# Performance work log

Hardware: AMD Instinct MI355X
Metric: run time of the kernel (lower is better)

The kernel has to match this reference:

```python
import jax, jax.numpy as jnp
import numpy as np

N_EXPERTS = 8
N_SHARED = 1
N_ROUTED = N_EXPERTS - N_SHARED          # 7
TOP_K_ROUTED = 3 - N_SHARED              # 2 routed experts per token
C = 1024
H = 4 * C


def _mlp(x, w_fc, w_proj):
    # x: [n, C]; w_fc: [C, H]; w_proj: [H, C]; exact (erf) GELU like torch nn.GELU
    return jax.nn.gelu(x @ w_fc, approximate=False) @ w_proj


def setup_inputs() -> dict:
    key = jax.random.key(0)
    ks = jax.random.split(key, 6)
    s = 0.02
    return {
        "x": jax.random.normal(ks[0], (4, 2048, C), dtype=jnp.float32),
        "gate_w": jax.random.normal(ks[1], (N_ROUTED, C), dtype=jnp.float32) * s,
        "lb_bias": jnp.zeros((N_ROUTED,), dtype=jnp.float32),
        "shared_wfc": jax.random.normal(ks[2], (C, H), dtype=jnp.float32) * s,
        "shared_wproj": jax.random.normal(ks[3], (H, C), dtype=jnp.float32) * s,
        "routed_wfc": jax.random.normal(ks[4], (N_ROUTED, C, H), dtype=jnp.float32) * s,
        "routed_wproj": jax.random.normal(ks[5], (N_ROUTED, H, C), dtype=jnp.float32) * s,
    }


def reference(x, gate_w, lb_bias, shared_wfc, shared_wproj, routed_wfc, routed_wproj):
    B, T, Cc = x.shape
    xt = x.reshape(-1, Cc)                       # [n, C]
    n = xt.shape[0]

    # shared expert(s) applied to every token
    shared_out = _mlp(xt, shared_wfc, shared_wproj)

    # routing
    routed_logits = xt @ gate_w.T                # [n, E_r]
    sel_logits = routed_logits + lb_bias
    _, topk_idx = jax.lax.top_k(sel_logits, TOP_K_ROUTED)   # [n, k]
    routed_probs = jax.nn.softmax(routed_logits.astype(jnp.float32), axis=-1)
    topk_w = jnp.take_along_axis(routed_probs, topk_idx, axis=-1)  # [n, k]

    # per-token combine weights over routed experts: [n, E_r]
    cw = jnp.zeros((n, N_ROUTED), dtype=jnp.float32)
    cw = cw.at[jnp.arange(n)[:, None], topk_idx].add(topk_w)

    # dispatch-combine: small fixed loop over routed experts
    routed_out = jnp.zeros_like(xt)
    for e in range(N_ROUTED):
        y = _mlp(xt, routed_wfc[e], routed_wproj[e])
        routed_out = routed_out + cw[:, e:e + 1] * y

    return (shared_out + routed_out).reshape(B, T, Cc)
```

## Files before the change

kernel.cpp:

```cpp
#include <hip/hip_runtime.h>
#include <hip/hip_bf16.h>

#define AS1 __attribute__((address_space(1)))
#define AS3 __attribute__((address_space(3)))

typedef __bf16 bf16x8 __attribute__((ext_vector_type(8)));
typedef float f32x4 __attribute__((ext_vector_type(4)));

static constexpr int C_DIM = 1024;
static constexpr int H_DIM = 4096;
static constexpr int NTOK  = 8192;
static constexpr int NR    = 7;
static constexpr int NSLOT = 17408;
static constexpr int MAXT  = 136;
static constexpr size_t WSZ = (size_t)C_DIM * H_DIM;

static __device__ __forceinline__ unsigned short f2bf(float f) {
  __hip_bfloat16 h = __float2bfloat16(f);
  return *reinterpret_cast<unsigned short*>(&h);
}
static __device__ __forceinline__ float bf2f(unsigned short u) {
  unsigned int v = ((unsigned int)u) << 16;
  return *reinterpret_cast<float*>(&v);
}

static __device__ __forceinline__ float gelu_fast(float v) {
  const float u2 = -2.0f * v * (0.7978845608f + 0.0356774081f * v * v);
  return v * __builtin_amdgcn_rcpf(1.0f + __expf(u2));
}

static __device__ __forceinline__ void gload16(const void* g, void* lds) {
  __builtin_amdgcn_global_load_lds((const AS1 void*)g, (AS3 void*)lds, 16, 0, 0);
}

__global__ __launch_bounds__(256) void cast_x_kernel(const float* __restrict__ x,
                                                     unsigned short* __restrict__ xb) {
  size_t i = ((size_t)blockIdx.x * blockDim.x + threadIdx.x) * 4;
  float4 v = *(const float4*)(x + i);
  ushort4 o;
  o.x = f2bf(v.x); o.y = f2bf(v.y); o.z = f2bf(v.z); o.w = f2bf(v.w);
  *(ushort4*)(xb + i) = o;
}

__global__ __launch_bounds__(256) void init_kernel(int* __restrict__ idx, int* __restrict__ cnt,
                                                   int* __restrict__ cursor) {
  int i = blockIdx.x * 256 + threadIdx.x;
  if (i < NSLOT) idx[i] = 0;
  if (blockIdx.x == 0 && threadIdx.x < 8) { cnt[threadIdx.x] = 0; cursor[threadIdx.x] = 0; }
}

__global__ __launch_bounds__(256) void routing_kernel(const float* __restrict__ x,
                                                      const float* __restrict__ gw,
                                                      const float* __restrict__ bias,
                                                      float* __restrict__ cw,
                                                      int* __restrict__ cnt) {
  int wid = (int)((blockIdx.x * (size_t)blockDim.x + threadIdx.x) >> 6);
  int lane = threadIdx.x & 63;
  if (wid >= NTOK) return;
  const float* xt = x + (size_t)wid * C_DIM;
  float p[NR] = {0.f, 0.f, 0.f, 0.f, 0.f, 0.f, 0.f};
  for (int i = lane; i < C_DIM; i += 64) {
    float xv = xt[i];
#pragma unroll
    for (int e = 0; e < NR; ++e) p[e] += xv * gw[e * C_DIM + i];
  }
#pragma unroll
  for (int e = 0; e < NR; ++e) {
#pragma unroll
    for (int off = 32; off; off >>= 1) p[e] += __shfl_down(p[e], off);
  }
  if (lane == 0) {
    float m = p[0];
#pragma unroll
    for (int e = 1; e < NR; ++e) m = fmaxf(m, p[e]);
    float pr[NR], s = 0.f;
#pragma unroll
    for (int e = 0; e < NR; ++e) { pr[e] = __expf(p[e] - m); s += pr[e]; }
    float inv = 1.0f / s;
#pragma unroll
    for (int e = 0; e < NR; ++e) pr[e] *= inv;
    float sel[NR];
#pragma unroll
    for (int e = 0; e < NR; ++e) sel[e] = p[e] + bias[e];
    int i1 = 0;
#pragma unroll
    for (int e = 1; e < NR; ++e) if (sel[e] > sel[i1]) i1 = e;
    int i2 = -1;
#pragma unroll
    for (int e = 0; e < NR; ++e) {
      if (e == i1) continue;
      if (i2 < 0 || sel[e] > sel[i2]) i2 = e;
    }
    float c[NR] = {0.f, 0.f, 0.f, 0.f, 0.f, 0.f, 0.f};
    c[i1] = pr[i1];
    c[i2] += pr[i2];
#pragma unroll
    for (int e = 0; e < NR; ++e) cw[(size_t)wid * NR + e] = c[e];
    atomicAdd(&cnt[i1], 1);
    atomicAdd(&cnt[i2], 1);
  }
}

__global__ void scan_kernel(const int* __restrict__ cnt, int* __restrict__ offs,
                            int* __restrict__ tmap, int* __restrict__ ntiles) {
  int o = 0, nt = 0;
  for (int e = 0; e < NR; ++e) {
    offs[e] = o;
    int n = (cnt[e] + 127) & ~127;
    o += n;
    for (int tm = 0; tm < n; tm += 128) tmap[nt++] = (e << 16) | tm;
  }
  *ntiles = nt;
}

__global__ __launch_bounds__(256) void place_kernel(const float* __restrict__ cw,
                                                    const int* __restrict__ offs,
                                                    int* __restrict__ cursor,
                                                    int* __restrict__ idx,
                                                    int* __restrict__ tok2slot,
                                                    float* __restrict__ tok2w) {
  int t = blockIdx.x * 256 + threadIdx.x;
  if (t >= NTOK) return;
  int k = 0;
#pragma unroll
  for (int e = 0; e < NR; ++e) {
    float w = cw[(size_t)t * NR + e];
    if (w > 0.f) {
      int p = atomicAdd(&cursor[e], 1);
      int slot = offs[e] + p;
      idx[slot] = t;
      tok2slot[t * 2 + k] = slot;
      tok2w[t * 2 + k] = w;
      ++k;
    }
  }
}

__global__ void transpose_cast_all(const float* __restrict__ shared_w,
                                   const float* __restrict__ routed_w,
                                   unsigned short* __restrict__ out, int R, int S) {
  int e = blockIdx.z;
  const float* in = (e == 0) ? shared_w : routed_w + (size_t)(e - 1) * R * S;
  unsigned short* o = out + (size_t)e * R * S;
  __shared__ float t[32][33];
  int bx = blockIdx.x * 32;
  int by = blockIdx.y * 32;
  int tx = threadIdx.x, ty = threadIdx.y;
#pragma unroll
  for (int i = 0; i < 32; i += 8)
    t[ty + i][tx] = in[(size_t)(by + ty + i) * S + bx + tx];
  __syncthreads();
#pragma unroll
  for (int i = 0; i < 32; i += 8)
    o[(size_t)(bx + ty + i) * R + by + tx] = f2bf(t[tx][ty + i]);
}


template <bool GATHER>
__global__ __launch_bounds__(256) void gemm_fc(const unsigned short* __restrict__ A,
                                               const unsigned short* __restrict__ BtAll,
                                               unsigned short* __restrict__ Y,
                                               const int* __restrict__ idx,
                                               const int* __restrict__ offs,
                                               const int* __restrict__ tmap,
                                               const int* __restrict__ ntiles) {
  __shared__ __align__(16) unsigned short As[3][4096];
  __shared__ __align__(16) unsigned short Bs[3][4096];
  const int tid = threadIdx.x;
  const int wave = tid >> 6, lane = tid & 63;
  constexpr int NT = C_DIM / 32;

  const int f = blockIdx.y * gridDim.x + blockIdx.x;
  const int cpx = (gridDim.x * gridDim.y) >> 3;
  const int swz = (f & 7) * cpx + (f >> 3);
  const int bx = swz % gridDim.x, ty = swz / gridDim.x;

  int m0, n0, base;
  const unsigned short* Bt;
  if (GATHER) {
    if (ty >= *ntiles) return;
    const int packed = tmap[ty];
    const int e = packed >> 16;
    m0 = packed & 0xffff;
    n0 = bx * 128;
    base = offs[e];
    Bt = BtAll + (size_t)(e + 1) * WSZ;
  } else {
    m0 = ty * 128;
    n0 = bx * 128;
    base = 0;
    Bt = BtAll;
  }

  const int q0 = wave * 128 + lane, q1 = q0 + 64;
  const int kg0 = q0 >> 7, r0 = q0 & 127;
  const int kg1 = q1 >> 7, r1 = q1 & 127;
  const size_t rowA0 = GATHER ? (size_t)idx[base + m0 + r0] : (size_t)(m0 + r0);
  const size_t rowA1 = GATHER ? (size_t)idx[base + m0 + r1] : (size_t)(m0 + r1);
  const unsigned short* gA0 = A + rowA0 * C_DIM + kg0 * 8;
  const unsigned short* gA1 = A + rowA1 * C_DIM + kg1 * 8;
  const unsigned short* gB0 = Bt + (size_t)(n0 + r0) * C_DIM + kg0 * 8;
  const unsigned short* gB1 = Bt + (size_t)(n0 + r1) * C_DIM + kg1 * 8;
  const int c0 = (wave * 2 + 0) * 512, c1 = (wave * 2 + 1) * 512;

  const int wr = wave >> 1, wc = wave & 1;
  const int fr = lane & 15, fq = lane >> 4;
  f32x4 acc[4][4] = {};

  asm volatile("s_waitcnt vmcnt(0)" ::: "memory");
  gload16(gA0, &As[0][c0]); gload16(gA1, &As[0][c1]);
  gload16(gB0, &Bs[0][c0]); gload16(gB1, &Bs[0][c1]);
  gload16(gA0 + 32, &As[1][c0]); gload16(gA1 + 32, &As[1][c1]);
  gload16(gB0 + 32, &Bs[1][c0]); gload16(gB1 + 32, &Bs[1][c1]);

  int rb = 0;
  for (int t = 0; t < NT; ++t) {
    if (t + 2 < NT) {
      const int wb = (rb >= 1) ? rb - 1 : 2;
      const int nk = (t + 2) * 32;
      gload16(gA0 + nk, &As[wb][c0]); gload16(gA1 + nk, &As[wb][c1]);
      gload16(gB0 + nk, &Bs[wb][c0]); gload16(gB1 + nk, &Bs[wb][c1]);
      asm volatile("s_waitcnt vmcnt(8)" ::: "memory");
    } else if (t + 1 < NT) {
      asm volatile("s_waitcnt vmcnt(4)" ::: "memory");
    } else {
      asm volatile("s_waitcnt vmcnt(0)" ::: "memory");
    }
    __builtin_amdgcn_s_barrier();
    bf16x8 af[4], bfr[4];
#pragma unroll
    for (int m = 0; m < 4; ++m)
      af[m] = *(const bf16x8*)&As[rb][fq * 1024 + (wr * 64 + m * 16 + fr) * 8];
#pragma unroll
    for (int n = 0; n < 4; ++n)
      bfr[n] = *(const bf16x8*)&Bs[rb][fq * 1024 + (wc * 64 + n * 16 + fr) * 8];
#pragma unroll
    for (int m = 0; m < 4; ++m)
#pragma unroll
      for (int n = 0; n < 4; ++n)
        acc[m][n] = __builtin_amdgcn_mfma_f32_16x16x32_bf16(af[m], bfr[n], acc[m][n], 0, 0, 0);
    __builtin_amdgcn_s_barrier();
    rb = (rb == 2) ? 0 : rb + 1;
  }

#pragma unroll
  for (int m = 0; m < 4; ++m)
#pragma unroll
    for (int n = 0; n < 4; ++n)
#pragma unroll
      for (int j = 0; j < 4; ++j) {
        const int row = m0 + wr * 64 + m * 16 + fq * 4 + j;
        const int col = n0 + wc * 64 + n * 16 + fr;
        const float g = gelu_fast(acc[m][n][j]);
        __builtin_nontemporal_store(f2bf(g), &Y[(size_t)(base + row) * H_DIM + col]);
      }
}

__global__ __launch_bounds__(256) void gemm_proj_shared(const unsigned short* __restrict__ Yg,
                                                        const unsigned short* __restrict__ Bt,
                                                        float* __restrict__ Out) {
  __shared__ __align__(16) unsigned short As[3][4096];
  __shared__ __align__(16) unsigned short Bs[3][4096];
  const int tid = threadIdx.x;
  const int wave = tid >> 6, lane = tid & 63;
  constexpr int NT = H_DIM / 32;

  const int f = blockIdx.y * gridDim.x + blockIdx.x;
  const int cpx = (gridDim.x * gridDim.y) >> 3;
  const int swz = (f & 7) * cpx + (f >> 3);
  const int m0 = (swz / gridDim.x) * 128;
  const int n0 = (swz % gridDim.x) * 128;

  const int q0 = wave * 128 + lane, q1 = q0 + 64;
  const int kg0 = q0 >> 7, r0 = q0 & 127;
  const int kg1 = q1 >> 7, r1 = q1 & 127;
  const unsigned short* gA0 = Yg + (size_t)(m0 + r0) * H_DIM + kg0 * 8;
  const unsigned short* gA1 = Yg + (size_t)(m0 + r1) * H_DIM + kg1 * 8;
  const unsigned short* gB0 = Bt + (size_t)(n0 + r0) * H_DIM + kg0 * 8;
  const unsigned short* gB1 = Bt + (size_t)(n0 + r1) * H_DIM + kg1 * 8;
  const int c0 = (wave * 2 + 0) * 512, c1 = (wave * 2 + 1) * 512;

  const int wr = wave >> 1, wc = wave & 1;
  const int fr = lane & 15, fq = lane >> 4;
  f32x4 acc[4][4] = {};

  gload16(gA0, &As[0][c0]); gload16(gA1, &As[0][c1]);
  gload16(gB0, &Bs[0][c0]); gload16(gB1, &Bs[0][c1]);
  gload16(gA0 + 32, &As[1][c0]); gload16(gA1 + 32, &As[1][c1]);
  gload16(gB0 + 32, &Bs[1][c0]); gload16(gB1 + 32, &Bs[1][c1]);

  int rb = 0;
  for (int t = 0; t < NT; ++t) {
    if (t + 2 < NT) {
      const int wb = (rb >= 1) ? rb - 1 : 2;
      const int nk = (t + 2) * 32;
      gload16(gA0 + nk, &As[wb][c0]); gload16(gA1 + nk, &As[wb][c1]);
      gload16(gB0 + nk, &Bs[wb][c0]); gload16(gB1 + nk, &Bs[wb][c1]);
      asm volatile("s_waitcnt vmcnt(8)" ::: "memory");
    } else if (t + 1 < NT) {
      asm volatile("s_waitcnt vmcnt(4)" ::: "memory");
    } else {
      asm volatile("s_waitcnt vmcnt(0)" ::: "memory");
    }
    __builtin_amdgcn_s_barrier();
    bf16x8 af[4], bfr[4];
#pragma unroll
    for (int m = 0; m < 4; ++m)
      af[m] = *(const bf16x8*)&As[rb][fq * 1024 + (wr * 64 + m * 16 + fr) * 8];
#pragma unroll
    for (int n = 0; n < 4; ++n)
      bfr[n] = *(const bf16x8*)&Bs[rb][fq * 1024 + (wc * 64 + n * 16 + fr) * 8];
#pragma unroll
    for (int m = 0; m < 4; ++m)
#pragma unroll
      for (int n = 0; n < 4; ++n)
        acc[m][n] = __builtin_amdgcn_mfma_f32_16x16x32_bf16(af[m], bfr[n], acc[m][n], 0, 0, 0);
    __builtin_amdgcn_s_barrier();
    rb = (rb == 2) ? 0 : rb + 1;
  }

#pragma unroll
  for (int m = 0; m < 4; ++m)
#pragma unroll
    for (int n = 0; n < 4; ++n)
#pragma unroll
      for (int j = 0; j < 4; ++j) {
        const int p = wr * 64 + m * 16 + fq * 4 + j;
        const int col = n0 + wc * 64 + n * 16 + fr;
        Out[(size_t)(m0 + p) * C_DIM + col] = acc[m][n][j];
      }
}

__global__ __launch_bounds__(256) void gemm_proj_routed(const unsigned short* __restrict__ Yg,
                                                        const unsigned short* __restrict__ BtAll,
                                                        unsigned short* __restrict__ Pb,
                                                        const int* __restrict__ offs,
                                                        const int* __restrict__ tmap,
                                                        const int* __restrict__ ntiles) {
  __shared__ __align__(16) unsigned short As[3][4096];
  __shared__ __align__(16) unsigned short Bs[3][4096];
  const int tid = threadIdx.x;
  const int wave = tid >> 6, lane = tid & 63;
  constexpr int KSEG = H_DIM / 2;
  constexpr int NT = KSEG / 32;
  const int kbase = blockIdx.z * KSEG;

  const int f = blockIdx.y * gridDim.x + blockIdx.x;
  const int cpx = (gridDim.x * gridDim.y) >> 3;
  const int swz = (f & 7) * cpx + (f >> 3);
  const int bx = swz % gridDim.x, ty = swz / gridDim.x;

  if (ty >= *ntiles) return;
  const int packed = tmap[ty];
  const int e = packed >> 16;
  const int m0 = packed & 0xffff;
  const int n0 = bx * 128;
  const int base = offs[e];
  const unsigned short* Bt = BtAll + (size_t)(e + 1) * WSZ;

  const int q0 = wave * 128 + lane, q1 = q0 + 64;
  const int kg0 = q0 >> 7, r0 = q0 & 127;
  const int kg1 = q1 >> 7, r1 = q1 & 127;
  const unsigned short* gA0 = Yg + (size_t)(base + m0 + r0) * H_DIM + kbase + kg0 * 8;
  const unsigned short* gA1 = Yg + (size_t)(base + m0 + r1) * H_DIM + kbase + kg1 * 8;
  const unsigned short* gB0 = Bt + (size_t)(n0 + r0) * H_DIM + kbase + kg0 * 8;
  const unsigned short* gB1 = Bt + (size_t)(n0 + r1) * H_DIM + kbase + kg1 * 8;
  const int c0 = (wave * 2 + 0) * 512, c1 = (wave * 2 + 1) * 512;

  const int wr = wave >> 1, wc = wave & 1;
  const int fr = lane & 15, fq = lane >> 4;
  f32x4 acc[4][4] = {};

  gload16(gA0, &As[0][c0]); gload16(gA1, &As[0][c1]);
  gload16(gB0, &Bs[0][c0]); gload16(gB1, &Bs[0][c1]);
  gload16(gA0 + 32, &As[1][c0]); gload16(gA1 + 32, &As[1][c1]);
  gload16(gB0 + 32, &Bs[1][c0]); gload16(gB1 + 32, &Bs[1][c1]);

  int rb = 0;
  for (int t = 0; t < NT; ++t) {
    if (t + 2 < NT) {
      const int wb = (rb >= 1) ? rb - 1 : 2;
      const int nk = (t + 2) * 32;
      gload16(gA0 + nk, &As[wb][c0]); gload16(gA1 + nk, &As[wb][c1]);
      gload16(gB0 + nk, &Bs[wb][c0]); gload16(gB1 + nk, &Bs[wb][c1]);
      asm volatile("s_waitcnt vmcnt(8)" ::: "memory");
    } else if (t + 1 < NT) {
      asm volatile("s_waitcnt vmcnt(4)" ::: "memory");
    } else {
      asm volatile("s_waitcnt vmcnt(0)" ::: "memory");
    }
    __builtin_amdgcn_s_barrier();
    bf16x8 af[4], bfr[4];
#pragma unroll
    for (int m = 0; m < 4; ++m)
      af[m] = *(const bf16x8*)&As[rb][fq * 1024 + (wr * 64 + m * 16 + fr) * 8];
#pragma unroll
    for (int n = 0; n < 4; ++n)
      bfr[n] = *(const bf16x8*)&Bs[rb][fq * 1024 + (wc * 64 + n * 16 + fr) * 8];
#pragma unroll
    for (int m = 0; m < 4; ++m)
#pragma unroll
      for (int n = 0; n < 4; ++n)
        acc[m][n] = __builtin_amdgcn_mfma_f32_16x16x32_bf16(af[m], bfr[n], acc[m][n], 0, 0, 0);
    __builtin_amdgcn_s_barrier();
    rb = (rb == 2) ? 0 : rb + 1;
  }

#pragma unroll
  for (int m = 0; m < 4; ++m)
#pragma unroll
    for (int n = 0; n < 4; ++n)
#pragma unroll
      for (int j = 0; j < 4; ++j) {
        const int p = wr * 64 + m * 16 + fq * 4 + j;
        const int col = n0 + wc * 64 + n * 16 + fr;
        __builtin_nontemporal_store(
            f2bf(acc[m][n][j]),
            &Pb[((size_t)blockIdx.z * NSLOT + base + m0 + p) * C_DIM + col]);
      }
}

__global__ __launch_bounds__(256) void combine_kernel(const unsigned short* __restrict__ P,
                                                      const int* __restrict__ tok2slot,
                                                      const float* __restrict__ tok2w,
                                                      float* __restrict__ out) {
  const int t = blockIdx.x;
  const int c = threadIdx.x * 4;
  const int s0 = tok2slot[t * 2], s1 = tok2slot[t * 2 + 1];
  const float w0 = tok2w[t * 2], w1 = tok2w[t * 2 + 1];
  const ushort4 a0 = *(const ushort4*)&P[((size_t)0 * NSLOT + s0) * C_DIM + c];
  const ushort4 a1 = *(const ushort4*)&P[((size_t)1 * NSLOT + s0) * C_DIM + c];
  const ushort4 b0 = *(const ushort4*)&P[((size_t)0 * NSLOT + s1) * C_DIM + c];
  const ushort4 b1 = *(const ushort4*)&P[((size_t)1 * NSLOT + s1) * C_DIM + c];
  float4 o = *(float4*)&out[(size_t)t * C_DIM + c];
  o.x += w0 * (bf2f(a0.x) + bf2f(a1.x)) + w1 * (bf2f(b0.x) + bf2f(b1.x));
  o.y += w0 * (bf2f(a0.y) + bf2f(a1.y)) + w1 * (bf2f(b0.y) + bf2f(b1.y));
  o.z += w0 * (bf2f(a0.z) + bf2f(a1.z)) + w1 * (bf2f(b0.z) + bf2f(b1.z));
  o.w += w0 * (bf2f(a0.w) + bf2f(a1.w)) + w1 * (bf2f(b0.w) + bf2f(b1.w));
  *(float4*)&out[(size_t)t * C_DIM + c] = o;
}

extern "C" void kernel_launch(void* const* d_in, const int* in_sizes, int n_in,
                              void* d_out, int out_size, void* d_ws, size_t ws_size,
                              hipStream_t stream) {
  const float* x            = (const float*)d_in[0];
  const float* gate_w       = (const float*)d_in[1];
  const float* lb_bias      = (const float*)d_in[2];
  const float* shared_wfc   = (const float*)d_in[3];
  const float* shared_wproj = (const float*)d_in[4];
  const float* routed_wfc   = (const float*)d_in[5];
  const float* routed_wproj = (const float*)d_in[6];
  float* out = (float*)d_out;

  char* ws = (char*)d_ws;
  unsigned short* xb     = (unsigned short*)(ws);
  unsigned short* wfcT   = (unsigned short*)(ws + 16777216);
  unsigned short* Pb     = (unsigned short*)(ws);
  unsigned short* wprojT = (unsigned short*)(ws + 83886080);
  unsigned short* Yg     = (unsigned short*)(ws + 150994944);
  float*          cw     = (float*)(ws + 293601280);
  int*            idx    = (int*)(ws + 293830656);
  int*            cnt    = (int*)(ws + 293901312);
  int*            offs   = (int*)(ws + 293901376);
  int*            cursor = (int*)(ws + 293901440);
  int*            tok2slot = (int*)(ws + 293901504);
  float*          tok2w    = (float*)(ws + 293967040);
  int*            tmap     = (int*)(ws + 294032576);
  int*            ntiles   = (int*)(ws + 294033152);

  cast_x_kernel<<<NTOK * C_DIM / (256 * 4), 256, 0, stream>>>(x, xb);
  init_kernel<<<(NSLOT + 255) / 256, 256, 0, stream>>>(idx, cnt, cursor);
  routing_kernel<<<NTOK / 4, 256, 0, stream>>>(x, gate_w, lb_bias, cw, cnt);
  scan_kernel<<<1, 1, 0, stream>>>(cnt, offs, tmap, ntiles);
  place_kernel<<<NTOK / 256, 256, 0, stream>>>(cw, offs, cursor, idx, tok2slot, tok2w);

  transpose_cast_all<<<dim3(H_DIM / 32, C_DIM / 32, 8), dim3(32, 8), 0, stream>>>(
      shared_wfc, routed_wfc, wfcT, C_DIM, H_DIM);
  transpose_cast_all<<<dim3(C_DIM / 32, H_DIM / 32, 8), dim3(32, 8), 0, stream>>>(
      shared_wproj, routed_wproj, wprojT, H_DIM, C_DIM);

  gemm_fc<false><<<dim3(H_DIM / 128, NTOK / 128), 256, 0, stream>>>(
      xb, wfcT, Yg, idx, offs, tmap, ntiles);
  gemm_proj_shared<<<dim3(C_DIM / 128, NTOK / 128), 256, 0, stream>>>(Yg, wprojT, out);

  gemm_fc<true><<<dim3(H_DIM / 128, MAXT), 256, 0, stream>>>(
      xb, wfcT, Yg, idx, offs, tmap, ntiles);
  gemm_proj_routed<<<dim3(C_DIM / 128, MAXT, 2), 256, 0, stream>>>(
      Yg, wprojT, Pb, offs, tmap, ntiles);

  combine_kernel<<<NTOK, 256, 0, stream>>>(Pb, tok2slot, tok2w, out);
}
```

Before: 1.276 ms.

## Use 256-row tiles with 512-thread blocks for fc and routed proj GEMMs

Moves the fc GEMM and the routed proj GEMM from 128x128 tiles with 256 threads to 256x128 tiles with 512 threads (8 waves), so each B tile loaded is reused across twice as many rows. The routed tile map now stores absolute slot offsets and a per-tile row limit, and stores are masked so a 256-row tile cannot spill into the next expert's slots. This halves the tile count per expert (MAXT drops to 76) and cuts weight traffic. The cost is more LDS per block, possible occupancy loss, and wasted work on partially filled 256-row tiles.

```diff
diff --git a/kernel.cpp b/kernel.cpp
--- a/kernel.cpp
+++ b/kernel.cpp
@@ -12,7 +12,7 @@
 static constexpr int NTOK  = 8192;
 static constexpr int NR    = 7;
 static constexpr int NSLOT = 17408;
-static constexpr int MAXT  = 136;
+static constexpr int MAXT  = 76;
 static constexpr size_t WSZ = (size_t)C_DIM * H_DIM;
 
 static __device__ __forceinline__ unsigned short f2bf(float f) {
@@ -102,13 +102,18 @@
 }
 
 __global__ void scan_kernel(const int* __restrict__ cnt, int* __restrict__ offs,
-                            int* __restrict__ tmap, int* __restrict__ ntiles) {
+                            int* __restrict__ tmap, int* __restrict__ tlim,
+                            int* __restrict__ ntiles) {
   int o = 0, nt = 0;
   for (int e = 0; e < NR; ++e) {
     offs[e] = o;
-    int n = (cnt[e] + 127) & ~127;
-    o += n;
-    for (int tm = 0; tm < n; tm += 128) tmap[nt++] = (e << 16) | tm;
+    int a = (cnt[e] + 127) & ~127;
+    for (int tm = 0; tm < a; tm += 256) {
+      tmap[nt] = ((e + 1) << 20) | (o + tm);
+      tlim[nt] = o + a;
+      ++nt;
+    }
+    o += a;
   }
   *ntiles = nt;
 }
@@ -157,57 +162,219 @@
 
 
 template <bool GATHER>
-__global__ __launch_bounds__(256) void gemm_fc(const unsigned short* __restrict__ A,
-                                               const unsigned short* __restrict__ BtAll,
-                                               unsigned short* __restrict__ Y,
-                                               const int* __restrict__ idx,
-                                               const int* __restrict__ offs,
-                                               const int* __restrict__ tmap,
-                                               const int* __restrict__ ntiles) {
+__global__ __launch_bounds__(512, 4) void gemm_fc(const unsigned short* __restrict__ A,
+                                                  const unsigned short* __restrict__ BtAll,
+                                                  unsigned short* __restrict__ Y,
+                                                  const int* __restrict__ idx,
+                                                  const int* __restrict__ tmap,
+                                                  const int* __restrict__ tlim,
+                                                  const int* __restrict__ ntiles) {
+  __shared__ __align__(16) unsigned short As[3][8192];
+  __shared__ __align__(16) unsigned short Bs[3][4096];
+  constexpr int K = C_DIM;
+  constexpr int NT = K / 32;
+  const int tid = threadIdx.x;
+  const int wave = tid >> 6, lane = tid & 63;
+
+  const int f = blockIdx.y * gridDim.x + blockIdx.x;
+  const int cpx = (gridDim.x * gridDim.y) >> 3;
+  const int swz = (f & 7) * cpx + (f >> 3);
+  const int bx = swz % gridDim.x, ty = swz / gridDim.x;
+
+  int m0, lim;
+  const unsigned short* Bt;
+  if (GATHER) {
+    if (ty >= *ntiles) return;
+    const int packed = tmap[ty];
+    m0 = packed & 0xfffff;
+    lim = tlim[ty];
+    Bt = BtAll + (size_t)(packed >> 20) * WSZ;
+  } else {
+    m0 = ty * 256;
+    lim = 1 << 30;
+    Bt = BtAll;
+  }
+  const int n0 = bx * 128;
+
+  const int rA = tid & 255, kgA = tid >> 8;
+  const int rB = tid & 127, kgB = tid >> 7;
+  int arow = m0 + rA;
+  if (GATHER) arow = idx[arow];
+  const unsigned short* gA = A + (size_t)arow * K;
+  const unsigned short* gB = Bt + (size_t)(n0 + rB) * K;
+  const int oA0 = kgA * 8, oA1 = (kgA + 2) * 8, oB = kgB * 8;
+  const int dA0 = wave * 512, dA1 = wave * 512 + 4096, dB = wave * 512;
+
+  const int wr = wave >> 1, wc = wave & 1;
+  const int fr = lane & 15, fq = lane >> 4;
+  f32x4 acc[4][4] = {};
+
+  asm volatile("s_waitcnt vmcnt(0)" ::: "memory");
+  gload16(gA + oA0, &As[0][dA0]); gload16(gA + oA1, &As[0][dA1]); gload16(gB + oB, &Bs[0][dB]);
+  gload16(gA + 32 + oA0, &As[1][dA0]); gload16(gA + 32 + oA1, &As[1][dA1]);
+  gload16(gB + 32 + oB, &Bs[1][dB]);
+
+  int rb = 0;
+  for (int t = 0; t < NT; ++t) {
+    if (t + 2 < NT) {
+      const int wb = (rb >= 1) ? rb - 1 : 2;
+      const int nk = (t + 2) * 32;
+      gload16(gA + nk + oA0, &As[wb][dA0]);
+      gload16(gA + nk + oA1, &As[wb][dA1]);
+      gload16(gB + nk + oB, &Bs[wb][dB]);
+      asm volatile("s_waitcnt vmcnt(6)" ::: "memory");
+    } else if (t + 1 < NT) {
+      asm volatile("s_waitcnt vmcnt(3)" ::: "memory");
+    } else {
+      asm volatile("s_waitcnt vmcnt(0)" ::: "memory");
+    }
+    __builtin_amdgcn_s_barrier();
+    bf16x8 af[4], bfr[4];
+#pragma unroll
+    for (int m = 0; m < 4; ++m)
+      af[m] = *(const bf16x8*)&As[rb][fq * 2048 + (wr * 64 + m * 16 + fr) * 8];
+#pragma unroll
+    for (int n = 0; n < 4; ++n)
+      bfr[n] = *(const bf16x8*)&Bs[rb][fq * 1024 + (wc * 64 + n * 16 + fr) * 8];
+#pragma unroll
+    for (int m = 0; m < 4; ++m)
+#pragma unroll
+      for (int n = 0; n < 4; ++n)
+        acc[m][n] = __builtin_amdgcn_mfma_f32_16x16x32_bf16(af[m], bfr[n], acc[m][n], 0, 0, 0);
+    __builtin_amdgcn_s_barrier();
+    rb = (rb == 2) ? 0 : rb + 1;
+  }
+
+#pragma unroll
+  for (int m = 0; m < 4; ++m)
+#pragma unroll
+    for (int n = 0; n < 4; ++n)
+#pragma unroll
+      for (int j = 0; j < 4; ++j) {
+        const int slot = m0 + wr * 64 + m * 16 + fq * 4 + j;
+        const int col = n0 + wc * 64 + n * 16 + fr;
+        if (!GATHER || slot < lim) {
+          const float g = gelu_fast(acc[m][n][j]);
+          Y[(size_t)slot * H_DIM + col] = f2bf(g);
+        }
+      }
+}
+
+__global__ __launch_bounds__(512, 4) void gemm_proj_routed(const unsigned short* __restrict__ Yg,
+                                                           const unsigned short* __restrict__ BtAll,
+                                                           unsigned short* __restrict__ Pb,
+                                                           const int* __restrict__ tmap,
+                                                           const int* __restrict__ tlim,
+                                                           const int* __restrict__ ntiles) {
+  __shared__ __align__(16) unsigned short As[3][8192];
+  __shared__ __align__(16) unsigned short Bs[3][4096];
+  constexpr int KSEG = H_DIM / 2;
+  constexpr int NT = KSEG / 32;
+  const int tid = threadIdx.x;
+  const int wave = tid >> 6, lane = tid & 63;
+  const int kbase = blockIdx.z * KSEG;
+
+  const int f = blockIdx.y * gridDim.x + blockIdx.x;
+  const int cpx = (gridDim.x * gridDim.y) >> 3;
+  const int swz = (f & 7) * cpx + (f >> 3);
+  const int bx = swz % gridDim.x, ty = swz / gridDim.x;
+
+  if (ty >= *ntiles) return;
+  const int packed = tmap[ty];
+  const int m0 = packed & 0xfffff;
+  const int lim = tlim[ty];
+  const unsigned short* Bt = BtAll + (size_t)(packed >> 20) * WSZ;
+  const int n0 = bx * 128;
+
+  const int rA = tid & 255, kgA = tid >> 8;
+  const int rB = tid & 127, kgB = tid >> 7;
+  const unsigned short* gA = Yg + (size_t)(m0 + rA) * H_DIM + kbase;
+  const unsigned short* gB = Bt + (size_t)(n0 + rB) * H_DIM + kbase;
+  const int oA0 = kgA * 8, oA1 = (kgA + 2) * 8, oB = kgB * 8;
+  const int dA0 = wave * 512, dA1 = wave * 512 + 4096, dB = wave * 512;
+
+  const int wr = wave >> 1, wc = wave & 1;
+  const int fr = lane & 15, fq = lane >> 4;
+  f32x4 acc[4][4] = {};
+
+  gload16(gA + oA0, &As[0][dA0]); gload16(gA + oA1, &As[0][dA1]); gload16(gB + oB, &Bs[0][dB]);
+  gload16(gA + 32 + oA0, &As[1][dA0]); gload16(gA + 32 + oA1, &As[1][dA1]);
+  gload16(gB + 32 + oB, &Bs[1][dB]);
+
+  int rb = 0;
+  for (int t = 0; t < NT; ++t) {
+    if (t + 2 < NT) {
+      const int wb = (rb >= 1) ? rb - 1 : 2;
+      const int nk = (t + 2) * 32;
+      gload16(gA + nk + oA0, &As[wb][dA0]);
+      gload16(gA + nk + oA1, &As[wb][dA1]);
+      gload16(gB + nk + oB, &Bs[wb][dB]);
+      asm volatile("s_waitcnt vmcnt(6)" ::: "memory");
+    } else if (t + 1 < NT) {
+      asm volatile("s_waitcnt vmcnt(3)" ::: "memory");
+    } else {
+      asm volatile("s_waitcnt vmcnt(0)" ::: "memory");
+    }
+    __builtin_amdgcn_s_barrier();
+    bf16x8 af[4], bfr[4];
+#pragma unroll
+    for (int m = 0; m < 4; ++m)
+      af[m] = *(const bf16x8*)&As[rb][fq * 2048 + (wr * 64 + m * 16 + fr) * 8];
+#pragma unroll
+    for (int n = 0; n < 4; ++n)
+      bfr[n] = *(const bf16x8*)&Bs[rb][fq * 1024 + (wc * 64 + n * 16 + fr) * 8];
+#pragma unroll
+    for (int m = 0; m < 4; ++m)
+#pragma unroll
+      for (int n = 0; n < 4; ++n)
+        acc[m][n] = __builtin_amdgcn_mfma_f32_16x16x32_bf16(af[m], bfr[n], acc[m][n], 0, 0, 0);
+    __builtin_amdgcn_s_barrier();
+    rb = (rb == 2) ? 0 : rb + 1;
+  }
+
+#pragma unroll
+  for (int m = 0; m < 4; ++m)
+#pragma unroll
+    for (int n = 0; n < 4; ++n)
+#pragma unroll
+      for (int j = 0; j < 4; ++j) {
+        const int slot = m0 + wr * 64 + m * 16 + fq * 4 + j;
+        const int col = n0 + wc * 64 + n * 16 + fr;
+        if (slot < lim)
+          __builtin_nontemporal_store(
+              f2bf(acc[m][n][j]),
+              &Pb[((size_t)blockIdx.z * NSLOT + slot) * C_DIM + col]);
+      }
+}
+
+__global__ __launch_bounds__(256) void gemm_proj_shared(const unsigned short* __restrict__ Yg,
+                                                        const unsigned short* __restrict__ Bt,
+                                                        float* __restrict__ Out) {
   __shared__ __align__(16) unsigned short As[3][4096];
   __shared__ __align__(16) unsigned short Bs[3][4096];
   const int tid = threadIdx.x;
   const int wave = tid >> 6, lane = tid & 63;
-  constexpr int NT = C_DIM / 32;
+  constexpr int NT = H_DIM / 32;
 
   const int f = blockIdx.y * gridDim.x + blockIdx.x;
   const int cpx = (gridDim.x * gridDim.y) >> 3;
   const int swz = (f & 7) * cpx + (f >> 3);
-  const int bx = swz % gridDim.x, ty = swz / gridDim.x;
-
-  int m0, n0, base;
-  const unsigned short* Bt;
-  if (GATHER) {
-    if (ty >= *ntiles) return;
-    const int packed = tmap[ty];
-    const int e = packed >> 16;
-    m0 = packed & 0xffff;
-    n0 = bx * 128;
-    base = offs[e];
-    Bt = BtAll + (size_t)(e + 1) * WSZ;
-  } else {
-    m0 = ty * 128;
-    n0 = bx * 128;
-    base = 0;
-    Bt = BtAll;
-  }
+  const int m0 = (swz / gridDim.x) * 128;
+  const int n0 = (swz % gridDim.x) * 128;
 
   const int q0 = wave * 128 + lane, q1 = q0 + 64;
   const int kg0 = q0 >> 7, r0 = q0 & 127;
   const int kg1 = q1 >> 7, r1 = q1 & 127;
-  const size_t rowA0 = GATHER ? (size_t)idx[base + m0 + r0] : (size_t)(m0 + r0);
-  const size_t rowA1 = GATHER ? (size_t)idx[base + m0 + r1] : (size_t)(m0 + r1);
-  const unsigned short* gA0 = A + rowA0 * C_DIM + kg0 * 8;
-  const unsigned short* gA1 = A + rowA1 * C_DIM + kg1 * 8;
-  const unsigned short* gB0 = Bt + (size_t)(n0 + r0) * C_DIM + kg0 * 8;
-  const unsigned short* gB1 = Bt + (size_t)(n0 + r1) * C_DIM + kg1 * 8;
+  const unsigned short* gA0 = Yg + (size_t)(m0 + r0) * H_DIM + kg0 * 8;
+  const unsigned short* gA1 = Yg + (size_t)(m0 + r1) * H_DIM + kg1 * 8;
+  const unsigned short* gB0 = Bt + (size_t)(n0 + r0) * H_DIM + kg0 * 8;
+  const unsigned short* gB1 = Bt + (size_t)(n0 + r1) * H_DIM + kg1 * 8;
   const int c0 = (wave * 2 + 0) * 512, c1 = (wave * 2 + 1) * 512;
 
   const int wr = wave >> 1, wc = wave & 1;
   const int fr = lane & 15, fq = lane >> 4;
   f32x4 acc[4][4] = {};
 
-  asm volatile("s_waitcnt vmcnt(0)" ::: "memory");
   gload16(gA0, &As[0][c0]); gload16(gA1, &As[0][c1]);
   gload16(gB0, &Bs[0][c0]); gload16(gB1, &Bs[0][c1]);
   gload16(gA0 + 32, &As[1][c0]); gload16(gA1 + 32, &As[1][c1]);
@@ -249,174 +416,9 @@
     for (int n = 0; n < 4; ++n)
 #pragma unroll
       for (int j = 0; j < 4; ++j) {
-        const int row = m0 + wr * 64 + m * 16 + fq * 4 + j;
-        const int col = n0 + wc * 64 + n * 16 + fr;
-        const float g = gelu_fast(acc[m][n][j]);
-        __builtin_nontemporal_store(f2bf(g), &Y[(size_t)(base + row) * H_DIM + col]);
-      }
-}
-
-__global__ __launch_bounds__(256) void gemm_proj_shared(const unsigned short* __restrict__ Yg,
-                                                        const unsigned short* __restrict__ Bt,
-                                                        float* __restrict__ Out) {
-  __shared__ __align__(16) unsigned short As[3][4096];
-  __shared__ __align__(16) unsigned short Bs[3][4096];
-  const int tid = threadIdx.x;
-  const int wave = tid >> 6, lane = tid & 63;
-  constexpr int NT = H_DIM / 32;
-
-  const int f = blockIdx.y * gridDim.x + blockIdx.x;
-  const int cpx = (gridDim.x * gridDim.y) >> 3;
-  const int swz = (f & 7) * cpx + (f >> 3);
-  const int m0 = (swz / gridDim.x) * 128;
-  const int n0 = (swz % gridDim.x) * 128;
-
-  const int q0 = wave * 128 + lane, q1 = q0 + 64;
-  const int kg0 = q0 >> 7, r0 = q0 & 127;
-  const int kg1 = q1 >> 7, r1 = q1 & 127;
-  const unsigned short* gA0 = Yg + (size_t)(m0 + r0) * H_DIM + kg0 * 8;
-  const unsigned short* gA1 = Yg + (size_t)(m0 + r1) * H_DIM + kg1 * 8;
-  const unsigned short* gB0 = Bt + (size_t)(n0 + r0) * H_DIM + kg0 * 8;
-  const unsigned short* gB1 = Bt + (size_t)(n0 + r1) * H_DIM + kg1 * 8;
-  const int c0 = (wave * 2 + 0) * 512, c1 = (wave * 2 + 1) * 512;
-
-  const int wr = wave >> 1, wc = wave & 1;
-  const int fr = lane & 15, fq = lane >> 4;
-  f32x4 acc[4][4] = {};
-
-  gload16(gA0, &As[0][c0]); gload16(gA1, &As[0][c1]);
-  gload16(gB0, &Bs[0][c0]); gload16(gB1, &Bs[0][c1]);
-  gload16(gA0 + 32, &As[1][c0]); gload16(gA1 + 32, &As[1][c1]);
-  gload16(gB0 + 32, &Bs[1][c0]); gload16(gB1 + 32, &Bs[1][c1]);
-
-  int rb = 0;
-  for (int t = 0; t < NT; ++t) {
-    if (t + 2 < NT) {
-      const int wb = (rb >= 1) ? rb - 1 : 2;
-      const int nk = (t + 2) * 32;
-      gload16(gA0 + nk, &As[wb][c0]); gload16(gA1 + nk, &As[wb][c1]);
-      gload16(gB0 + nk, &Bs[wb][c0]); gload16(gB1 + nk, &Bs[wb][c1]);
-      asm volatile("s_waitcnt vmcnt(8)" ::: "memory");
-    } else if (t + 1 < NT) {
-      asm volatile("s_waitcnt vmcnt(4)" ::: "memory");
-    } else {
-      asm volatile("s_waitcnt vmcnt(0)" ::: "memory");
-    }
-    __builtin_amdgcn_s_barrier();
-    bf16x8 af[4], bfr[4];
-#pragma unroll
-    for (int m = 0; m < 4; ++m)
-      af[m] = *(const bf16x8*)&As[rb][fq * 1024 + (wr * 64 + m * 16 + fr) * 8];
-#pragma unroll
-    for (int n = 0; n < 4; ++n)
-      bfr[n] = *(const bf16x8*)&Bs[rb][fq * 1024 + (wc * 64 + n * 16 + fr) * 8];
-#pragma unroll
-    for (int m = 0; m < 4; ++m)
-#pragma unroll
-      for (int n = 0; n < 4; ++n)
-        acc[m][n] = __builtin_amdgcn_mfma_f32_16x16x32_bf16(af[m], bfr[n], acc[m][n], 0, 0, 0);
-    __builtin_amdgcn_s_barrier();
-    rb = (rb == 2) ? 0 : rb + 1;
-  }
-
-#pragma unroll
-  for (int m = 0; m < 4; ++m)
-#pragma unroll
-    for (int n = 0; n < 4; ++n)
-#pragma unroll
-      for (int j = 0; j < 4; ++j) {
         const int p = wr * 64 + m * 16 + fq * 4 + j;
         const int col = n0 + wc * 64 + n * 16 + fr;
         Out[(size_t)(m0 + p) * C_DIM + col] = acc[m][n][j];
-      }
-}
-
-__global__ __launch_bounds__(256) void gemm_proj_routed(const unsigned short* __restrict__ Yg,
-                                                        const unsigned short* __restrict__ BtAll,
-                                                        unsigned short* __restrict__ Pb,
-                                                        const int* __restrict__ offs,
-                                                        const int* __restrict__ tmap,
-                                                        const int* __restrict__ ntiles) {
-  __shared__ __align__(16) unsigned short As[3][4096];
-  __shared__ __align__(16) unsigned short Bs[3][4096];
-  const int tid = threadIdx.x;
-  const int wave = tid >> 6, lane = tid & 63;
-  constexpr int KSEG = H_DIM / 2;
-  constexpr int NT = KSEG / 32;
-  const int kbase = blockIdx.z * KSEG;
-
-  const int f = blockIdx.y * gridDim.x + blockIdx.x;
-  const int cpx = (gridDim.x * gridDim.y) >> 3;
-  const int swz = (f & 7) * cpx + (f >> 3);
-  const int bx = swz % gridDim.x, ty = swz / gridDim.x;
-
-  if (ty >= *ntiles) return;
-  const int packed = tmap[ty];
-  const int e = packed >> 16;
-  const int m0 = packed & 0xffff;
-  const int n0 = bx * 128;
-  const int base = offs[e];
-  const unsigned short* Bt = BtAll + (size_t)(e + 1) * WSZ;
-
-  const int q0 = wave * 128 + lane, q1 = q0 + 64;
-  const int kg0 = q0 >> 7, r0 = q0 & 127;
-  const int kg1 = q1 >> 7, r1 = q1 & 127;
-  const unsigned short* gA0 = Yg + (size_t)(base + m0 + r0) * H_DIM + kbase + kg0 * 8;
-  const unsigned short* gA1 = Yg + (size_t)(base + m0 + r1) * H_DIM + kbase + kg1 * 8;
-  const unsigned short* gB0 = Bt + (size_t)(n0 + r0) * H_DIM + kbase + kg0 * 8;
-  const unsigned short* gB1 = Bt + (size_t)(n0 + r1) * H_DIM + kbase + kg1 * 8;
-  const int c0 = (wave * 2 + 0) * 512, c1 = (wave * 2 + 1) * 512;
-
-  const int wr = wave >> 1, wc = wave & 1;
-  const int fr = lane & 15, fq = lane >> 4;
-  f32x4 acc[4][4] = {};
-
-  gload16(gA0, &As[0][c0]); gload16(gA1, &As[0][c1]);
-  gload16(gB0, &Bs[0][c0]); gload16(gB1, &Bs[0][c1]);
-  gload16(gA0 + 32, &As[1][c0]); gload16(gA1 + 32, &As[1][c1]);
-  gload16(gB0 + 32, &Bs[1][c0]); gload16(gB1 + 32, &Bs[1][c1]);
-
-  int rb = 0;
-  for (int t = 0; t < NT; ++t) {
-    if (t + 2 < NT) {
-      const int wb = (rb >= 1) ? rb - 1 : 2;
-      const int nk = (t + 2) * 32;
-      gload16(gA0 + nk, &As[wb][c0]); gload16(gA1 + nk, &As[wb][c1]);
-      gload16(gB0 + nk, &Bs[wb][c0]); gload16(gB1 + nk, &Bs[wb][c1]);
-      asm volatile("s_waitcnt vmcnt(8)" ::: "memory");
-    } else if (t + 1 < NT) {
-      asm volatile("s_waitcnt vmcnt(4)" ::: "memory");
-    } else {
-      asm volatile("s_waitcnt vmcnt(0)" ::: "memory");
-    }
-    __builtin_amdgcn_s_barrier();
-    bf16x8 af[4], bfr[4];
-#pragma unroll
-    for (int m = 0; m < 4; ++m)
-      af[m] = *(const bf16x8*)&As[rb][fq * 1024 + (wr * 64 + m * 16 + fr) * 8];
-#pragma unroll
-    for (int n = 0; n < 4; ++n)
-      bfr[n] = *(const bf16x8*)&Bs[rb][fq * 1024 + (wc * 64 + n * 16 + fr) * 8];
-#pragma unroll
-    for (int m = 0; m < 4; ++m)
-#pragma unroll
-      for (int n = 0; n < 4; ++n)
-        acc[m][n] = __builtin_amdgcn_mfma_f32_16x16x32_bf16(af[m], bfr[n], acc[m][n], 0, 0, 0);
-    __builtin_amdgcn_s_barrier();
-    rb = (rb == 2) ? 0 : rb + 1;
-  }
-
-#pragma unroll
-  for (int m = 0; m < 4; ++m)
-#pragma unroll
-    for (int n = 0; n < 4; ++n)
-#pragma unroll
-      for (int j = 0; j < 4; ++j) {
-        const int p = wr * 64 + m * 16 + fq * 4 + j;
-        const int col = n0 + wc * 64 + n * 16 + fr;
-        __builtin_nontemporal_store(
-            f2bf(acc[m][n][j]),
-            &Pb[((size_t)blockIdx.z * NSLOT + base + m0 + p) * C_DIM + col]);
       }
 }
 
@@ -466,12 +468,13 @@
   int*            tok2slot = (int*)(ws + 293901504);
   float*          tok2w    = (float*)(ws + 293967040);
   int*            tmap     = (int*)(ws + 294032576);
-  int*            ntiles   = (int*)(ws + 294033152);
+  int*            tlim     = (int*)(ws + 294032960);
+  int*            ntiles   = (int*)(ws + 294033344);
 
   cast_x_kernel<<<NTOK * C_DIM / (256 * 4), 256, 0, stream>>>(x, xb);
   init_kernel<<<(NSLOT + 255) / 256, 256, 0, stream>>>(idx, cnt, cursor);
   routing_kernel<<<NTOK / 4, 256, 0, stream>>>(x, gate_w, lb_bias, cw, cnt);
-  scan_kernel<<<1, 1, 0, stream>>>(cnt, offs, tmap, ntiles);
+  scan_kernel<<<1, 1, 0, stream>>>(cnt, offs, tmap, tlim, ntiles);
   place_kernel<<<NTOK / 256, 256, 0, stream>>>(cw, offs, cursor, idx, tok2slot, tok2w);
 
   transpose_cast_all<<<dim3(H_DIM / 32, C_DIM / 32, 8), dim3(32, 8), 0, stream>>>(
@@ -479,14 +482,14 @@
   transpose_cast_all<<<dim3(C_DIM / 32, H_DIM / 32, 8), dim3(32, 8), 0, stream>>>(
       shared_wproj, routed_wproj, wprojT, H_DIM, C_DIM);
 
-  gemm_fc<false><<<dim3(H_DIM / 128, NTOK / 128), 256, 0, stream>>>(
-      xb, wfcT, Yg, idx, offs, tmap, ntiles);
+  gemm_fc<false><<<dim3(H_DIM / 128, NTOK / 256), 512, 0, stream>>>(
+      xb, wfcT, Yg, idx, tmap, tlim, ntiles);
   gemm_proj_shared<<<dim3(C_DIM / 128, NTOK / 128), 256, 0, stream>>>(Yg, wprojT, out);
 
-  gemm_fc<true><<<dim3(H_DIM / 128, MAXT), 256, 0, stream>>>(
-      xb, wfcT, Yg, idx, offs, tmap, ntiles);
-  gemm_proj_routed<<<dim3(C_DIM / 128, MAXT, 2), 256, 0, stream>>>(
-      Yg, wprojT, Pb, offs, tmap, ntiles);
+  gemm_fc<true><<<dim3(H_DIM / 128, MAXT), 512, 0, stream>>>(
+      xb, wfcT, Yg, idx, tmap, tlim, ntiles);
+  gemm_proj_routed<<<dim3(C_DIM / 128, MAXT, 2), 512, 0, stream>>>(
+      Yg, wprojT, Pb, tmap, tlim, ntiles);
 
   combine_kernel<<<NTOK, 256, 0, stream>>>(Pb, tok2slot, tok2w, out);
 }
```

Measured after the change: 1.377 ms. 1.08x slower.
